# Optimization experiments

Measured on AMD Instinct MI355X. Metric: run time of the kernel, lower is better.

Reference implementation:

```python
import jax, jax.numpy as jnp
import numpy as np

TEMPERATURE = 0.5
EPS = 1e-8  # torch F.cosine_similarity eps


def _neg_mask_indices(two_b):
    """Static row/col indices replicating sim[mask].view(2B, -1).
    Mask excludes the diagonal and the (i, B+i)/(B+i, i) positive pairs,
    leaving exactly 2B-2 entries per row, extracted in row-major order."""
    b = two_b // 2
    mask = np.ones((two_b, two_b), dtype=bool)
    np.fill_diagonal(mask, False)
    i = np.arange(b)
    mask[i, b + i] = False
    mask[b + i, i] = False
    rows, cols = np.nonzero(mask)
    return rows.reshape(two_b, two_b - 2), cols.reshape(two_b, two_b - 2)


def setup_inputs() -> dict:
    key = jax.random.key(0)
    k1, k2 = jax.random.split(key)
    two_b, d = 8192, 128
    embeddings = jax.random.normal(k1, (two_b, d), dtype=jnp.float32)
    labels = jax.random.randint(k2, (two_b,), 0, two_b - 2)
    return {"embeddings": embeddings, "labels": labels}


def reference(embeddings, labels):
    two_b = embeddings.shape[0]
    # cosine similarity via normalize + matmul (same math as the broadcast
    # F.cosine_similarity, without the O(N^2*D) intermediate)
    norms = jnp.linalg.norm(embeddings, axis=1)  # [2B]
    sim = (embeddings @ embeddings.T) / jnp.maximum(norms[:, None] * norms[None, :], EPS)
    sim = sim / TEMPERATURE  # [2B, 2B]
    rows, cols = _neg_mask_indices(two_b)
    logits = sim[rows, cols]  # [2B, 2B-2]
    # CrossEntropyLoss(reduction='sum') then / (2B)
    logz = jax.nn.logsumexp(logits, axis=1)  # [2B]
    picked = jnp.take_along_axis(logits, labels[:, None].astype(jnp.int32), axis=1)[:, 0]
    loss = jnp.sum(logz - picked) / two_b
    return loss
```

## Files before the change

kernel.cpp:

```cpp
#include <hip/hip_runtime.h>
#include <hip/hip_bf16.h>


typedef __bf16 bf16x8 __attribute__((ext_vector_type(8)));
typedef float floatx4 __attribute__((ext_vector_type(4)));

#define TWO_B 8192
#define B_HALF 4096
#define D 128
#define INV_T 2.0f
#define FIXED_MAX 2.0f
#define C_EXP 2.885390081777927f
#define NSPLIT 16
#define NROWBLK (TWO_B / 128)

#if defined(__has_builtin) && __has_builtin(__builtin_amdgcn_exp2f)
#define EXP2F(x) __builtin_amdgcn_exp2f(x)
#else
#define EXP2F(x) exp2f(x)
#endif
#if defined(__has_builtin) && __has_builtin(__builtin_amdgcn_logf)
#define LOG2F(x) __builtin_amdgcn_logf(x)
#else
#define LOG2F(x) log2f(x)
#endif

__device__ inline void load16_lds(const __bf16* g, __bf16* l) {
    __builtin_amdgcn_global_load_lds(
        (const __attribute__((address_space(1))) unsigned int*)g,
        (__attribute__((address_space(3))) unsigned int*)l, 16, 0, 0);
}

__global__ void k_prep(const float* __restrict__ emb,
                       const int* __restrict__ labels,
                       __bf16* __restrict__ nb,
                       float* __restrict__ picked,
                       float* __restrict__ l_arr) {
    int wv   = threadIdx.x >> 6;
    int lane = threadIdx.x & 63;
    int i = blockIdx.x * 4 + wv;
    const float2* e2 = reinterpret_cast<const float2*>(emb + (size_t)i * D);
    float2 v = e2[lane];
    float ssi = v.x * v.x + v.y * v.y;
    int p = i ^ B_HALF;
    int a = min(i, p), b = max(i, p);
    int l = labels[i];
    int c = l + (l >= a);
    c += (c >= b);
    const float2* ec2 = reinterpret_cast<const float2*>(emb + (size_t)c * D);
    float2 u = ec2[lane];
    float dot = v.x * u.x + v.y * u.y;
    float ssc = u.x * u.x + u.y * u.y;
#pragma unroll
    for (int off = 32; off >= 1; off >>= 1) {
        ssi += __shfl_xor(ssi, off, 64);
        dot += __shfl_xor(dot, off, 64);
        ssc += __shfl_xor(ssc, off, 64);
    }
    float rn = rsqrtf(fmaxf(ssi, 1e-16f));
    union { __bf16 h[2]; unsigned int uu; } pk;
    pk.h[0] = (__bf16)(v.x * rn);
    pk.h[1] = (__bf16)(v.y * rn);
    reinterpret_cast<unsigned int*>(nb)[i * 64 + lane] = pk.uu;
    if (lane == 0)
        picked[i] = dot / fmaxf(sqrtf(ssi * ssc), 1e-8f) * INV_T;
    if (blockIdx.x < TWO_B / 256) l_arr[blockIdx.x * 256 + threadIdx.x] = 0.f;
}

__global__ __launch_bounds__(256, 4) void k_gemm(const __bf16* __restrict__ nb,
                                                 float* __restrict__ l_arr) {
    __shared__ __bf16 lds[16384];

    const int lane = threadIdx.x & 63;
    const int w    = threadIdx.x >> 6;
    const int m    = lane & 15;
    const int quad = lane >> 4;
    const int row0 = blockIdx.x * 128 + w * 32;
    const int colB = blockIdx.y * 512;

    const int r0 = blockIdx.x * 128;
    const int pr0 = r0 ^ B_HALF;
    const bool bmask = ((r0 < colB + 512) && (colB < r0 + 128)) ||
                       ((pr0 < colB + 512) && (colB < pr0 + 128));

    bf16x8 a0[4], a1[4];
#pragma unroll
    for (int kc = 0; kc < 4; ++kc) {
        a0[kc] = *reinterpret_cast<const bf16x8*>(
            nb + (size_t)(row0 + m) * D + kc * 32 + quad * 8);
        a1[kc] = *reinterpret_cast<const bf16x8*>(
            nb + (size_t)(row0 + 16 + m) * D + kc * 32 + quad * 8);
    }
    asm volatile("" : "+v"(a0[0]), "+v"(a0[1]), "+v"(a0[2]), "+v"(a0[3]),
                      "+v"(a1[0]), "+v"(a1[1]), "+v"(a1[2]), "+v"(a1[3]));

    float l0[4] = {0.f, 0.f, 0.f, 0.f};
    float l1[4] = {0.f, 0.f, 0.f, 0.f};
    const int i0 = row0 + quad * 4;

    for (int ch = 0; ch < 4; ++ch) {
        const int colbase = colB + ch * 128;
        {
            const __bf16* g = nb + (size_t)(colbase + m) * D + w * 32 + quad * 8;
#pragma unroll
            for (int j = 0; j < 8; ++j)
                load16_lds(g + (size_t)j * 16 * D, &lds[j * 2048 + w * 512]);
        }
        __syncthreads();

#pragma unroll
        for (int grp = 0; grp < 2; ++grp) {
            floatx4 acc0[4] = {{0.f,0.f,0.f,0.f},{0.f,0.f,0.f,0.f},
                               {0.f,0.f,0.f,0.f},{0.f,0.f,0.f,0.f}};
            floatx4 acc1[4] = {{0.f,0.f,0.f,0.f},{0.f,0.f,0.f,0.f},
                               {0.f,0.f,0.f,0.f},{0.f,0.f,0.f,0.f}};
#pragma unroll
            for (int kc = 0; kc < 4; ++kc) {
                const bf16x8 a0k = a0[kc], a1k = a1[kc];
#pragma unroll
                for (int s = 0; s < 4; ++s) {
                    bf16x8 b = *reinterpret_cast<const bf16x8*>(
                        &lds[((grp * 4 + s) * 4 + kc) * 512 + lane * 8]);
                    acc0[s] = __builtin_amdgcn_mfma_f32_16x16x32_bf16(a0k, b, acc0[s], 0, 0, 0);
                    acc1[s] = __builtin_amdgcn_mfma_f32_16x16x32_bf16(a1k, b, acc1[s], 0, 0, 0);
                }
            }
#pragma unroll
            for (int s = 0; s < 4; ++s) {
                const int jj = colbase + (grp * 4 + s) * 16 + m;
                if (bmask) {
#pragma unroll
                    for (int r = 0; r < 4; ++r) {
                        float e0 = EXP2F(fmaf(acc0[s][r], C_EXP, -C_EXP));
                        float e1 = EXP2F(fmaf(acc1[s][r], C_EXP, -C_EXP));
                        if (((jj ^ (i0 + r)) & ~B_HALF) == 0) e0 = 0.f;
                        if (((jj ^ (i0 + 16 + r)) & ~B_HALF) == 0) e1 = 0.f;
                        l0[r] += e0;
                        l1[r] += e1;
                    }
                } else {
#pragma unroll
                    for (int r = 0; r < 4; ++r) {
                        l0[r] += EXP2F(fmaf(acc0[s][r], C_EXP, -C_EXP));
                        l1[r] += EXP2F(fmaf(acc1[s][r], C_EXP, -C_EXP));
                    }
                }
            }
        }
        __syncthreads();
    }

#pragma unroll
    for (int r = 0; r < 4; ++r) {
        float s = l0[r];
        s += __shfl_xor(s, 1, 64);
        s += __shfl_xor(s, 2, 64);
        s += __shfl_xor(s, 4, 64);
        s += __shfl_xor(s, 8, 64);
        if (m == 0) atomicAdd(&l_arr[i0 + r], s);
    }
#pragma unroll
    for (int r = 0; r < 4; ++r) {
        float s = l1[r];
        s += __shfl_xor(s, 1, 64);
        s += __shfl_xor(s, 2, 64);
        s += __shfl_xor(s, 4, 64);
        s += __shfl_xor(s, 8, 64);
        if (m == 0) atomicAdd(&l_arr[i0 + 16 + r], s);
    }
}

__global__ void k_final(const float* __restrict__ l_arr,
                        const float* __restrict__ picked,
                        float* __restrict__ out) {
    __shared__ float sred[4];
    float s = 0.f;
#pragma unroll
    for (int k = 0; k < TWO_B / 256; ++k) {
        int i = threadIdx.x + k * 256;
        s += FIXED_MAX + LOG2F(l_arr[i]) * 0.6931471805599453f - picked[i];
    }
#pragma unroll
    for (int off = 32; off >= 1; off >>= 1) s += __shfl_xor(s, off, 64);
    if ((threadIdx.x & 63) == 0) sred[threadIdx.x >> 6] = s;
    __syncthreads();
    if (threadIdx.x == 0)
        out[0] = (sred[0] + sred[1] + sred[2] + sred[3]) * (1.0f / TWO_B);
}

extern "C" void kernel_launch(void* const* d_in, const int* in_sizes, int n_in,
                              void* d_out, int out_size, void* d_ws, size_t ws_size,
                              hipStream_t stream) {
    const float* emb    = (const float*)d_in[0];
    const int*   labels = (const int*)d_in[1];
    char* ws = (char*)d_ws;
    float*  l_arr  = (float*)ws;
    float*  picked = (float*)(ws + 32768);
    __bf16* nb     = (__bf16*)(ws + 65536);
    float*  out    = (float*)d_out;

    k_prep<<<TWO_B / 4, 256, 0, stream>>>(emb, labels, nb, picked, l_arr);
    dim3 g2(NROWBLK, NSPLIT);
    k_gemm<<<g2, 256, 0, stream>>>(nb, l_arr);
    k_final<<<1, 256, 0, stream>>>(l_arr, picked, out);
}
```

Before: 91.57 us.

## Exploit symmetry of similarity matrix to compute only upper-triangular tiles

Each block now handles one 128x128 tile in a cyclic upper-triangle schedule, and off-diagonal tiles add their exp sums to both the row sums and the column sums via an LDS reduction plus atomics. This roughly halves the MFMA and exp work of the full 8192x8192 similarity. The cost is extra column reductions, more atomics, and many small one-tile blocks, some of which exit immediately. The by==32 tiles hold the positive-pair offset, where masking applies.

```diff
diff --git a/kernel.cpp b/kernel.cpp
--- a/kernel.cpp
+++ b/kernel.cpp
@@ -11,8 +11,6 @@
 #define INV_T 2.0f
 #define FIXED_MAX 2.0f
 #define C_EXP 2.885390081777927f
-#define NSPLIT 16
-#define NROWBLK (TWO_B / 128)
 
 #if defined(__has_builtin) && __has_builtin(__builtin_amdgcn_exp2f)
 #define EXP2F(x) __builtin_amdgcn_exp2f(x)
@@ -71,17 +69,20 @@
                                                  float* __restrict__ l_arr) {
     __shared__ __bf16 lds[16384];
 
+    const int bi = blockIdx.x;
+    const int by = blockIdx.y;
+    if (by == 32 && bi >= 32) return;
+    const int bj = (bi + by) & 63;
+    const int R0 = bi * 128;
+    const int C0 = bj * 128;
+    const bool isdiag = (by == 0);
+    const bool bmask = isdiag || (by == 32);
+
     const int lane = threadIdx.x & 63;
     const int w    = threadIdx.x >> 6;
     const int m    = lane & 15;
     const int quad = lane >> 4;
-    const int row0 = blockIdx.x * 128 + w * 32;
-    const int colB = blockIdx.y * 512;
-
-    const int r0 = blockIdx.x * 128;
-    const int pr0 = r0 ^ B_HALF;
-    const bool bmask = ((r0 < colB + 512) && (colB < r0 + 128)) ||
-                       ((pr0 < colB + 512) && (colB < pr0 + 128));
+    const int row0 = R0 + w * 32;
 
     bf16x8 a0[4], a1[4];
 #pragma unroll
@@ -94,60 +95,65 @@
     asm volatile("" : "+v"(a0[0]), "+v"(a0[1]), "+v"(a0[2]), "+v"(a0[3]),
                       "+v"(a1[0]), "+v"(a1[1]), "+v"(a1[2]), "+v"(a1[3]));
 
+    {
+        const __bf16* g = nb + (size_t)(C0 + m) * D + w * 32 + quad * 8;
+#pragma unroll
+        for (int j = 0; j < 8; ++j)
+            load16_lds(g + (size_t)j * 16 * D, &lds[j * 2048 + w * 512]);
+    }
+    __syncthreads();
+
     float l0[4] = {0.f, 0.f, 0.f, 0.f};
     float l1[4] = {0.f, 0.f, 0.f, 0.f};
+    float csum[8];
     const int i0 = row0 + quad * 4;
 
-    for (int ch = 0; ch < 4; ++ch) {
-        const int colbase = colB + ch * 128;
-        {
-            const __bf16* g = nb + (size_t)(colbase + m) * D + w * 32 + quad * 8;
-#pragma unroll
-            for (int j = 0; j < 8; ++j)
-                load16_lds(g + (size_t)j * 16 * D, &lds[j * 2048 + w * 512]);
-        }
-        __syncthreads();
-
-#pragma unroll
-        for (int grp = 0; grp < 2; ++grp) {
-            floatx4 acc0[4] = {{0.f,0.f,0.f,0.f},{0.f,0.f,0.f,0.f},
-                               {0.f,0.f,0.f,0.f},{0.f,0.f,0.f,0.f}};
-            floatx4 acc1[4] = {{0.f,0.f,0.f,0.f},{0.f,0.f,0.f,0.f},
-                               {0.f,0.f,0.f,0.f},{0.f,0.f,0.f,0.f}};
-#pragma unroll
-            for (int kc = 0; kc < 4; ++kc) {
-                const bf16x8 a0k = a0[kc], a1k = a1[kc];
-#pragma unroll
-                for (int s = 0; s < 4; ++s) {
-                    bf16x8 b = *reinterpret_cast<const bf16x8*>(
-                        &lds[((grp * 4 + s) * 4 + kc) * 512 + lane * 8]);
-                    acc0[s] = __builtin_amdgcn_mfma_f32_16x16x32_bf16(a0k, b, acc0[s], 0, 0, 0);
-                    acc1[s] = __builtin_amdgcn_mfma_f32_16x16x32_bf16(a1k, b, acc1[s], 0, 0, 0);
+#pragma unroll
+    for (int grp = 0; grp < 2; ++grp) {
+        floatx4 acc0[4] = {{0.f,0.f,0.f,0.f},{0.f,0.f,0.f,0.f},
+                           {0.f,0.f,0.f,0.f},{0.f,0.f,0.f,0.f}};
+        floatx4 acc1[4] = {{0.f,0.f,0.f,0.f},{0.f,0.f,0.f,0.f},
+                           {0.f,0.f,0.f,0.f},{0.f,0.f,0.f,0.f}};
+#pragma unroll
+        for (int kc = 0; kc < 4; ++kc) {
+            const bf16x8 a0k = a0[kc], a1k = a1[kc];
+#pragma unroll
+            for (int s = 0; s < 4; ++s) {
+                bf16x8 b = *reinterpret_cast<const bf16x8*>(
+                    &lds[((grp * 4 + s) * 4 + kc) * 512 + lane * 8]);
+                acc0[s] = __builtin_amdgcn_mfma_f32_16x16x32_bf16(a0k, b, acc0[s], 0, 0, 0);
+                acc1[s] = __builtin_amdgcn_mfma_f32_16x16x32_bf16(a1k, b, acc1[s], 0, 0, 0);
+            }
+        }
+#pragma unroll
+        for (int s = 0; s < 4; ++s) {
+            const int jj = C0 + (grp * 4 + s) * 16 + m;
+            float cs = 0.f;
+            if (bmask) {
+#pragma unroll
+                for (int r = 0; r < 4; ++r) {
+                    float e0 = EXP2F(fmaf(acc0[s][r], C_EXP, -C_EXP));
+                    float e1 = EXP2F(fmaf(acc1[s][r], C_EXP, -C_EXP));
+                    if (((jj ^ (i0 + r)) & ~B_HALF) == 0) e0 = 0.f;
+                    if (((jj ^ (i0 + 16 + r)) & ~B_HALF) == 0) e1 = 0.f;
+                    l0[r] += e0;
+                    l1[r] += e1;
+                    cs += e0 + e1;
+                }
+            } else {
+#pragma unroll
+                for (int r = 0; r < 4; ++r) {
+                    float e0 = EXP2F(fmaf(acc0[s][r], C_EXP, -C_EXP));
+                    float e1 = EXP2F(fmaf(acc1[s][r], C_EXP, -C_EXP));
+                    l0[r] += e0;
+                    l1[r] += e1;
+                    cs += e0 + e1;
                 }
             }
-#pragma unroll
-            for (int s = 0; s < 4; ++s) {
-                const int jj = colbase + (grp * 4 + s) * 16 + m;
-                if (bmask) {
-#pragma unroll
-                    for (int r = 0; r < 4; ++r) {
-                        float e0 = EXP2F(fmaf(acc0[s][r], C_EXP, -C_EXP));
-                        float e1 = EXP2F(fmaf(acc1[s][r], C_EXP, -C_EXP));
-                        if (((jj ^ (i0 + r)) & ~B_HALF) == 0) e0 = 0.f;
-                        if (((jj ^ (i0 + 16 + r)) & ~B_HALF) == 0) e1 = 0.f;
-                        l0[r] += e0;
-                        l1[r] += e1;
-                    }
-                } else {
-#pragma unroll
-                    for (int r = 0; r < 4; ++r) {
-                        l0[r] += EXP2F(fmaf(acc0[s][r], C_EXP, -C_EXP));
-                        l1[r] += EXP2F(fmaf(acc1[s][r], C_EXP, -C_EXP));
-                    }
-                }
-            }
-        }
-        __syncthreads();
+            cs += __shfl_xor(cs, 16, 64);
+            cs += __shfl_xor(cs, 32, 64);
+            csum[grp * 4 + s] = cs;
+        }
     }
 
 #pragma unroll
@@ -167,6 +173,22 @@
         s += __shfl_xor(s, 4, 64);
         s += __shfl_xor(s, 8, 64);
         if (m == 0) atomicAdd(&l_arr[i0 + 16 + r], s);
+    }
+
+    if (!isdiag) {
+        __syncthreads();
+        float* ldsf = reinterpret_cast<float*>(lds);
+        if (quad == 0) {
+#pragma unroll
+            for (int sub = 0; sub < 8; ++sub)
+                ldsf[w * 128 + sub * 16 + m] = csum[sub];
+        }
+        __syncthreads();
+        if (threadIdx.x < 128) {
+            float t = ldsf[threadIdx.x] + ldsf[128 + threadIdx.x] +
+                      ldsf[256 + threadIdx.x] + ldsf[384 + threadIdx.x];
+            atomicAdd(&l_arr[C0 + threadIdx.x], t);
+        }
     }
 }
 
@@ -200,7 +222,7 @@
     float*  out    = (float*)d_out;
 
     k_prep<<<TWO_B / 4, 256, 0, stream>>>(emb, labels, nb, picked, l_arr);
-    dim3 g2(NROWBLK, NSPLIT);
+    dim3 g2(64, 33);
     k_gemm<<<g2, 256, 0, stream>>>(nb, l_arr);
     k_final<<<1, 256, 0, stream>>>(l_arr, picked, out);
 }
```

Result: faster. 84.01 us (-8.3%).
